# Optimization experiments

Hardware: AMD Instinct MI355X
Metric: run time of the kernel (lower is better)

Reference implementation:

```python
import jax, jax.numpy as jnp
import numpy as np

B, S, F_DIM, FILT = 4096, 41, 128, 128
EPS_BN = 1e-5
EPS_SQ = 1e-21


def squash(v):
    n = jnp.linalg.norm(v, axis=-1, keepdims=True)
    return (1.0 - 1.0 / (jnp.exp(n) + EPS_SQ)) * (v / (n + EPS_SQ))


def position_linear(x, Wstack, bstack, window):
    # x: [B,S,F]; Wstack: [S, window*F, FILT]; bstack: [S, FILT]
    p = window // 2
    Bq, Sq, Fq = x.shape
    xp = jnp.pad(x, ((0, 0), (p, p), (0, 0)))
    idx = jnp.arange(Sq)[:, None] + jnp.arange(window)[None, :]  # [S, window]
    xw = xp[:, idx, :].reshape(Bq, Sq, window * Fq)
    return jax.nn.relu(jnp.einsum('bsf,sfo->bso', xw, Wstack) + bstack[None])


def batchnorm(x, g, b, axes):
    mu = jnp.mean(x, axis=axes, keepdims=True)
    var = jnp.var(x, axis=axes, keepdims=True)
    shape = [1] * x.ndim
    shape[1] = x.shape[1]
    return (x - mu) * jax.lax.rsqrt(var + EPS_BN) * g.reshape(shape) + b.reshape(shape)


def conv1d(x, w, groups=1):
    # x: [N,C,L], w: [O, C//groups, K], padding same (k=3, pad=1)
    return jax.lax.conv_general_dilated(
        x, w, window_strides=(1,), padding=[(1, 1)],
        dimension_numbers=('NCH', 'OIH', 'NCH'), feature_group_count=groups)


def setup_inputs() -> dict:
    key = jax.random.key(0)
    ks = jax.random.split(key, 16)
    sc = lambda fan_in: 1.0 / np.sqrt(fan_in)
    d = {}
    d['x'] = jax.random.randint(ks[0], (B, S), 0, 4, dtype=jnp.int32)
    d['emb'] = jax.random.normal(ks[1], (4, F_DIM), dtype=jnp.float32)
    for i, w in enumerate([3, 5, 7]):
        fin = w * F_DIM
        d[f'W{w}'] = jax.random.uniform(ks[2 + i], (S, fin, FILT), jnp.float32, -sc(fin), sc(fin))
        d[f'b{w}'] = jnp.zeros((S, FILT), jnp.float32)
    d['conv1_w'] = jax.random.uniform(ks[5], (64, 41, 3), jnp.float32, -sc(41 * 3), sc(41 * 3))
    d['conv1_b'] = jnp.zeros((64,), jnp.float32)
    d['bn_g'] = jnp.ones((64,), jnp.float32)
    d['bn_b'] = jnp.zeros((64,), jnp.float32)
    d['caps_w'] = jax.random.uniform(ks[6], (64, 32, 3), jnp.float32, -sc(32 * 3), sc(32 * 3))
    d['caps_b'] = jnp.zeros((64,), jnp.float32)
    d['route_W'] = jax.random.normal(ks[7], (2, 64, F_DIM), jnp.float32)
    d['route_b'] = jnp.zeros((2, 64, 1), jnp.float32)
    d['fc1_w'] = jax.random.uniform(ks[8], (F_DIM, 64), jnp.float32, -sc(F_DIM), sc(F_DIM))
    d['bn1_g'] = jnp.ones((2,), jnp.float32)
    d['bn1_b'] = jnp.zeros((2,), jnp.float32)
    d['fc2_w'] = jax.random.uniform(ks[9], (64, 32), jnp.float32, -sc(64), sc(64))
    d['bn2_g'] = jnp.ones((2,), jnp.float32)
    d['bn2_b'] = jnp.zeros((2,), jnp.float32)
    d['fc3_w'] = jax.random.uniform(ks[10], (32, 1), jnp.float32, -sc(32), sc(32))
    return d


def reference(x, emb, W3, b3, W5, b5, W7, b7, conv1_w, conv1_b, bn_g, bn_b,
              caps_w, caps_b, route_W, route_b,
              fc1_w, bn1_g, bn1_b, fc2_w, bn2_g, bn2_b, fc3_w):
    h = emb[x]                                    # [B,41,128]
    h = position_linear(h, W3, b3, 3)
    h = position_linear(h, W5, b5, 5)
    h = position_linear(h, W7, b7, 7)             # [B,41,128]
    h = conv1d(h, conv1_w) + conv1_b[None, :, None]  # [B,64,128]
    h = jax.nn.relu(batchnorm(h, bn_g, bn_b, axes=(0, 2)))
    h = conv1d(h, caps_w, groups=2) + caps_b[None, :, None]
    h = squash(h)                                 # [B,64,128]
    # Routing layer
    u = h[:, None, :, :] * route_W[None]          # [B,2,64,128]
    c = jnp.sum(u * u, axis=-1, keepdims=True) / jnp.sqrt(128.0)  # [B,2,64,1]
    c = jax.nn.softmax(c, axis=-1)                # softmax over size-1 axis -> ones
    c = c + route_b[None]
    s = squash(jnp.sum(u * c, axis=-2))           # [B,2,128]
    # FC head
    pair = s[:, :, None, :] + s[:, None, :, :]    # [B,2,2,128]
    y = jnp.max(pair, axis=1)                     # [B,2,128]
    y = jax.nn.relu(batchnorm(y @ fc1_w, bn1_g, bn1_b, axes=(0, 2)))
    y = jax.nn.relu(batchnorm(y @ fc2_w, bn2_g, bn2_b, axes=(0, 2)))
    y = jax.nn.sigmoid(y @ fc3_w)                 # [B,2,1]
    return jnp.max(y, axis=1)                     # [B,1]
```

## Files before the change

### kernel.cpp

```cpp
#include <hip/hip_runtime.h>
#include <cstdint>

typedef unsigned short u16;
typedef unsigned int   u32;
typedef __attribute__((ext_vector_type(8))) short bf16x8;
typedef __attribute__((ext_vector_type(4))) float f32x4;

#define DEVFN static __device__ __forceinline__

constexpr int B  = 4096;
constexpr int SQ = 41;

DEVFN float bf2f(u16 v) { return __uint_as_float(((u32)v) << 16); }
DEVFN u16 f2bf(float f) {
  u32 u = __float_as_uint(f);
  u += 0x7fffu + ((u >> 16) & 1u);
  return (u16)(u >> 16);
}
DEVFN u32 pack2(float a, float b) { return (u32)f2bf(a) | ((u32)f2bf(b) << 16); }

DEVFN void gload16(const void* g, void* l) {
  __builtin_amdgcn_global_load_lds(
      (const __attribute__((address_space(1))) unsigned int*)g,
      (__attribute__((address_space(3))) unsigned int*)l, 16, 0, 0);
}

__global__ void k_pack(const float* __restrict__ cw, const float* __restrict__ cpw,
                       const float* __restrict__ rW, const float* __restrict__ rb,
                       u16* __restrict__ wpk, u16* __restrict__ cpk,
                       u16* __restrict__ rwp) {
  int i = blockIdx.x * 256 + threadIdx.x;
  if (i < 12288) {
    int tt = i >> 12, rem = i & 4095, o = rem >> 6, c = rem & 63;
    float v = (c < 41) ? cw[(o * 41 + c) * 3 + tt] : 0.f;
    wpk[(tt * 64 + o) * 64 + (c ^ ((o & 7) << 3))] = f2bf(v);
  } else if (i < 18432) {
    int k = i - 12288;
    int tt = k >> 11, rem = k & 2047, o = rem >> 5, c = rem & 31;
    cpk[(tt * 64 + o) * 32 + (c ^ ((o & 3) << 3))] = f2bf(cpw[(o * 32 + c) * 3 + tt]);
  } else if (i < 34816) {
    int k = i - 18432;
    rwp[k] = f2bf(rW[k] * (1.f + rb[k >> 7]));
  }
}

__global__ void k_combo(const int* __restrict__ x, int* __restrict__ combo) {
  int i = blockIdx.x * 256 + threadIdx.x;
  if (i >= B * SQ) return;
  int b = i / SQ, s = i - b * SQ;
  const int* xb = x + b * SQ;
  int d0 = (s > 0) ? xb[s - 1] : 4;
  int d1 = xb[s];
  int d2 = (s < SQ - 1) ? xb[s + 1] : 4;
  combo[i] = d0 * 25 + d1 * 5 + d2;
}

__global__ void k_gmat(const float* __restrict__ emb, const float* __restrict__ W3,
                       float* __restrict__ G) {
  int s = blockIdx.x / 3, ww = blockIdx.x % 3;
  int o = threadIdx.x;
  const float* Ws = W3 + ((size_t)s * 384 + ww * 128) * 128;
  float a0 = 0.f, a1 = 0.f, a2 = 0.f, a3 = 0.f;
  for (int f = 0; f < 128; ++f) {
    float wg = Ws[(size_t)f * 128 + o];
    a0 = fmaf(emb[f], wg, a0);
    a1 = fmaf(emb[128 + f], wg, a1);
    a2 = fmaf(emb[256 + f], wg, a2);
    a3 = fmaf(emb[384 + f], wg, a3);
  }
  float* Gp = G + ((size_t)(s * 3 + ww) * 5) * 128 + o;
  Gp[0] = a0; Gp[128] = a1; Gp[256] = a2; Gp[384] = a3; Gp[512] = 0.f;
}

__global__ void k_t1(const float* __restrict__ G, const float* __restrict__ b3,
                     float* __restrict__ t1T) {
  int i = blockIdx.x * 256 + threadIdx.x;
  if (i >= SQ * 128 * 125) return;
  int v = i % 125, so = i / 125;
  int s = so >> 7, o = so & 127;
  int d0 = v / 25, r = v % 25;
  int d1 = r / 5, d2 = r % 5;
  float acc = b3[so]
      + G[((size_t)(s * 3 + 0) * 5 + d0) * 128 + o]
      + G[((size_t)(s * 3 + 1) * 5 + d1) * 128 + o]
      + G[((size_t)(s * 3 + 2) * 5 + d2) * 128 + o];
  t1T[i] = fmaxf(acc, 0.f);
}

__global__ __launch_bounds__(128) void k_t2(const float* __restrict__ t1T,
                                            const float* __restrict__ W5,
                                            u16* __restrict__ t2) {
  int bx = blockIdx.x;
  int s = bx / 25; int r = bx % 25;
  int ww = r / 5;  int vt = (r % 5) * 25;
  int o = threadIdx.x;
  int t = s + ww - 2;
  u16* dst = t2 + ((size_t)(s * 5 + ww) * 125 + vt) * 128 + o;
  if (t < 0 || t >= SQ) {
    #pragma unroll
    for (int v = 0; v < 25; ++v) dst[(size_t)v * 128] = 0;
    return;
  }
  float acc[25];
  #pragma unroll
  for (int v = 0; v < 25; ++v) acc[v] = 0.f;
  const float* Ws = W5 + ((size_t)s * 640 + ww * 128) * 128;
  const float* tp = t1T + (size_t)t * 128 * 125 + vt;
  for (int f = 0; f < 128; ++f) {
    float wg = Ws[(size_t)f * 128 + o];
    #pragma unroll
    for (int v = 0; v < 25; ++v) acc[v] = fmaf(tp[f * 125 + v], wg, acc[v]);
  }
  #pragma unroll
  for (int v = 0; v < 25; ++v) dst[(size_t)v * 128] = f2bf(acc[v]);
}

__global__ __launch_bounds__(256) void k_h2(const u16* __restrict__ t2,
                                            const int* __restrict__ combo,
                                            const float* __restrict__ b5,
                                            u16* __restrict__ h2) {
  const int i = blockIdx.x * 256 + threadIdx.x;
  const int o8 = (i & 15) * 8;
  const int rid = i >> 4;
  const int s = rid >> 12, b = rid & 4095;
  float acc[8];
  {
    float4 b0 = *reinterpret_cast<const float4*>(b5 + s * 128 + o8);
    float4 b1 = *reinterpret_cast<const float4*>(b5 + s * 128 + o8 + 4);
    acc[0] = b0.x; acc[1] = b0.y; acc[2] = b0.z; acc[3] = b0.w;
    acc[4] = b1.x; acc[5] = b1.y; acc[6] = b1.z; acc[7] = b1.w;
  }
  const int* cb = combo + b * SQ;
  #pragma unroll
  for (int ww = 0; ww < 5; ++ww) {
    const int t = s + ww - 2;
    if (0 <= t && t < SQ) {
      const int c = cb[t];
      uint4 raw = *reinterpret_cast<const uint4*>(
          t2 + ((size_t)(s * 5 + ww) * 125 + c) * 128 + o8);
      acc[0] += __uint_as_float(raw.x << 16);
      acc[1] += __uint_as_float(raw.x & 0xffff0000u);
      acc[2] += __uint_as_float(raw.y << 16);
      acc[3] += __uint_as_float(raw.y & 0xffff0000u);
      acc[4] += __uint_as_float(raw.z << 16);
      acc[5] += __uint_as_float(raw.z & 0xffff0000u);
      acc[6] += __uint_as_float(raw.w << 16);
      acc[7] += __uint_as_float(raw.w & 0xffff0000u);
    }
  }
  uint4 pk;
  pk.x = pack2(fmaxf(acc[0], 0.f), fmaxf(acc[1], 0.f));
  pk.y = pack2(fmaxf(acc[2], 0.f), fmaxf(acc[3], 0.f));
  pk.z = pack2(fmaxf(acc[4], 0.f), fmaxf(acc[5], 0.f));
  pk.w = pack2(fmaxf(acc[6], 0.f), fmaxf(acc[7], 0.f));
  *reinterpret_cast<uint4*>(h2 + ((size_t)b * SQ + s) * 128 + o8) = pk;
}

__global__ __launch_bounds__(256) void k_w7t(const float* __restrict__ W7,
                                             u16* __restrict__ w7t) {
  __shared__ float tile[64][65];
  const int s = blockIdx.z;
  const int k0 = blockIdx.x * 64;
  const int o0 = blockIdx.y * 64;
  const int t = threadIdx.x;
  #pragma unroll
  for (int i = 0; i < 16; ++i) {
    int idx = t + i * 256;
    int kl = idx >> 6, ol = idx & 63;
    tile[kl][ol] = W7[((size_t)s * 896 + k0 + kl) * 128 + o0 + ol];
  }
  __syncthreads();
  #pragma unroll
  for (int i = 0; i < 16; ++i) {
    int idx = t + i * 256;
    int ol = idx >> 6, kl = idx & 63;
    w7t[((size_t)s * 128 + o0 + ol) * 896 + k0 + kl] = f2bf(tile[kl][ol]);
  }
}

__global__ __launch_bounds__(256) void k_gemm7_mfma(const u16* __restrict__ h2,
                                                    const u16* __restrict__ w7t,
                                                    const float* __restrict__ b7,
                                                    u16* __restrict__ h3) {
  __shared__ u16 As[128 * 64];
  __shared__ u16 Bs[128 * 64];
  const int s  = blockIdx.y;
  const int b0 = blockIdx.x * 128;
  const int t  = threadIdx.x;
  const int lane = t & 63, w = t >> 6;
  const int wr = w >> 1, wc = w & 1;
  const int lcol = lane & 15, qk = lane >> 4;

  f32x4 acc[4][4];
  #pragma unroll
  for (int i = 0; i < 4; ++i)
    #pragma unroll
    for (int j = 0; j < 4; ++j) acc[i][j] = (f32x4){0.f, 0.f, 0.f, 0.f};

  const u16* wbase = w7t + (size_t)s * 128 * 896;

  for (int k0 = 0; k0 < 896; k0 += 64) {
    const int ww = k0 >> 7;
    const int tr = s + ww - 3;
    const int kf0 = k0 & 127;
    if (0 <= tr && tr < SQ) {
      #pragma unroll
      for (int it = 0; it < 4; ++it) {
        const int L = it * 4096 + t * 16;
        const int r = L >> 7;
        const int g = (L >> 4) & 7;
        const int gs = g ^ (r & 7);
        gload16(h2 + ((size_t)(b0 + r) * SQ + tr) * 128 + kf0 + gs * 8,
                (char*)As + it * 4096 + w * 1024);
      }
    } else {
      #pragma unroll
      for (int it = 0; it < 4; ++it)
        *reinterpret_cast<uint4*>((char*)As + it * 4096 + t * 16) =
            make_uint4(0u, 0u, 0u, 0u);
    }
    #pragma unroll
    for (int it = 0; it < 4; ++it) {
      const int L = it * 4096 + t * 16;
      const int o = L >> 7;
      const int g = (L >> 4) & 7;
      const int gs = g ^ (o & 7);
      gload16(wbase + (size_t)o * 896 + k0 + gs * 8,
              (char*)Bs + it * 4096 + w * 1024);
    }
    __syncthreads();
    #pragma unroll
    for (int kk = 0; kk < 2; ++kk) {
      const int gk = kk * 4 + qk;
      bf16x8 av[4], bv[4];
      #pragma unroll
      for (int m = 0; m < 4; ++m) {
        const int zr = wr * 64 + m * 16 + lcol;
        av[m] = *reinterpret_cast<const bf16x8*>(As + zr * 64 + ((gk ^ (zr & 7)) << 3));
      }
      #pragma unroll
      for (int n = 0; n < 4; ++n) {
        const int br = wc * 64 + n * 16 + lcol;
        bv[n] = *reinterpret_cast<const bf16x8*>(Bs + br * 64 + ((gk ^ (br & 7)) << 3));
      }
      #pragma unroll
      for (int m = 0; m < 4; ++m)
        #pragma unroll
        for (int n = 0; n < 4; ++n)
          acc[m][n] = __builtin_amdgcn_mfma_f32_16x16x32_bf16(av[m], bv[n], acc[m][n], 0, 0, 0);
    }
    __syncthreads();
  }

  const int rq = (lane >> 4) * 4;
  #pragma unroll
  for (int n = 0; n < 4; ++n) {
    const int o = wc * 64 + n * 16 + lcol;
    const float bias = b7[s * 128 + o];
    #pragma unroll
    for (int m = 0; m < 4; ++m) {
      #pragma unroll
      for (int rg = 0; rg < 4; ++rg) {
        const int row = b0 + wr * 64 + m * 16 + rq + rg;
        h3[((size_t)row * SQ + s) * 128 + o] = f2bf(fmaxf(acc[m][n][rg] + bias, 0.f));
      }
    }
  }
}

__global__ __launch_bounds__(256) void k_conv1(const u16* __restrict__ h3,
                                               const u16* __restrict__ wpk,
                                               const float* __restrict__ cb,
                                               u16* __restrict__ c1T,
                                               float2* __restrict__ part) {
  __shared__ u16 zs[6144];
  __shared__ u16 zt[130 * 64];
  __shared__ u16 wl[3 * 64 * 64];
  __shared__ float2 red[4][64];
  const int b = blockIdx.x;
  const int t = threadIdx.x;
  const int lane = t & 63, wv = t >> 6;

  const u16* src = h3 + (size_t)b * (SQ * 128);
  #pragma unroll
  for (int it = 0; it < 3; ++it)
    gload16(src + ((size_t)it * 256 + t) * 8, (char*)zs + it * 4096 + wv * 1024);
  #pragma unroll
  for (int it = 0; it < 6; ++it)
    gload16(wpk + ((size_t)it * 256 + t) * 8, (char*)wl + it * 4096 + wv * 1024);

  if (t < 64) zt[t] = 0;
  else if (t < 128) zt[129 * 64 + t - 64] = 0;
  __syncthreads();

  {
    const int l = t & 127, jb = (t >> 7) * 32;
    const int sw = ((l + 1) & 7) << 3;
    u16* dst = zt + (l + 1) * 64;
    #pragma unroll
    for (int j = 0; j < 32; ++j) {
      int c = (jb + j + l) & 63;
      dst[c ^ sw] = (c < 41) ? zs[c * 128 + l] : (u16)0;
    }
  }
  __syncthreads();

  f32x4 acc[2][4];
  #pragma unroll
  for (int m = 0; m < 2; ++m)
    #pragma unroll
    for (int n = 0; n < 4; ++n) acc[m][n] = (f32x4){0.f, 0.f, 0.f, 0.f};
  const int r = lane & 15, kq = (lane >> 4) * 8;

  #pragma unroll
  for (int tt = 0; tt < 3; ++tt) {
    #pragma unroll
    for (int kk = 0; kk < 2; ++kk) {
      const int kof = kk * 32 + kq;
      bf16x8 av[2], bv[4];
      #pragma unroll
      for (int m = 0; m < 2; ++m) {
        const int zr = wv * 32 + m * 16 + r + tt;
        av[m] = *reinterpret_cast<const bf16x8*>(zt + zr * 64 + (kof ^ ((zr & 7) << 3)));
      }
      #pragma unroll
      for (int n = 0; n < 4; ++n) {
        const int o = n * 16 + r;
        bv[n] = *reinterpret_cast<const bf16x8*>(wl + (tt * 64 + o) * 64 + (kof ^ ((o & 7) << 3)));
      }
      #pragma unroll
      for (int m = 0; m < 2; ++m)
        #pragma unroll
        for (int n = 0; n < 4; ++n)
          acc[m][n] = __builtin_amdgcn_mfma_f32_16x16x32_bf16(av[m], bv[n], acc[m][n], 0, 0, 0);
    }
  }

  const int q = lane >> 4;
  u16* outb = c1T + (size_t)b * 8192;
  #pragma unroll
  for (int n = 0; n < 4; ++n) {
    const int o = n * 16 + r;
    const float bias = cb[o];
    float s1 = 0.f, s2 = 0.f;
    #pragma unroll
    for (int m = 0; m < 2; ++m) {
      #pragma unroll
      for (int rg = 0; rg < 4; ++rg) {
        float v = acc[m][n][rg] + bias;
        s1 += v; s2 += v * v;
        outb[(wv * 32 + m * 16 + q * 4 + rg) * 64 + o] = f2bf(v);
      }
    }
    s1 += __shfl_xor(s1, 16); s1 += __shfl_xor(s1, 32);
    s2 += __shfl_xor(s2, 16); s2 += __shfl_xor(s2, 32);
    if (lane < 16) red[wv][n * 16 + lane] = make_float2(s1, s2);
  }
  __syncthreads();
  if (t < 64) {
    float S = red[0][t].x + red[1][t].x + red[2][t].x + red[3][t].x;
    float Q = red[0][t].y + red[1][t].y + red[2][t].y + red[3][t].y;
    part[(size_t)t * B + b] = make_float2(S, Q);
  }
}

__global__ void k_bnfin(const float2* __restrict__ part, const float* __restrict__ g,
                        const float* __restrict__ bb, float* __restrict__ scale,
                        float* __restrict__ shift) {
  int o = blockIdx.x;
  float s = 0.f, q = 0.f;
  for (int i = threadIdx.x; i < B; i += 256) {
    float2 p = part[(size_t)o * B + i];
    s += p.x; q += p.y;
  }
  #pragma unroll
  for (int off = 32; off; off >>= 1) { s += __shfl_down(s, off); q += __shfl_down(q, off); }
  __shared__ float rs[4], rq[4];
  int wv = threadIdx.x >> 6, ln = threadIdx.x & 63;
  if (ln == 0) { rs[wv] = s; rq[wv] = q; }
  __syncthreads();
  if (threadIdx.x == 0) {
    float S = rs[0] + rs[1] + rs[2] + rs[3];
    float Q = rq[0] + rq[1] + rq[2] + rq[3];
    const float n = (float)B * 128.f;
    float mu = S / n, var = Q / n - mu * mu;
    float sc = g[o] * rsqrtf(var + 1e-5f);
    scale[o] = sc; shift[o] = bb[o] - mu * sc;
  }
}

constexpr int NB = 8;
__global__ __launch_bounds__(256) void k_caps(const u16* __restrict__ c1T,
                                              const float* __restrict__ scale,
                                              const float* __restrict__ shift,
                                              const u16* __restrict__ cpk,
                                              const float* __restrict__ cpb,
                                              const u16* __restrict__ rwp,
                                              const float* __restrict__ f1,
                                              float* __restrict__ y1) {
  __shared__ u16 zt[130 * 64];
  __shared__ u16 wl[3 * 64 * 32];
  __shared__ float f1l[128 * 64];
  __shared__ float red[4][64];
  __shared__ float fl[64];
  __shared__ float sc_s[64], sh_s[64];
  __shared__ float red2[4][2];
  __shared__ float yl[2][128];
  __shared__ float pt[128];
  const int b0 = blockIdx.x * NB;
  const int t = threadIdx.x;
  const int lane = t & 63, wv = t >> 6;
  const int r = lane & 15, kq = (lane >> 4) * 8, q = lane >> 4;

  #pragma unroll
  for (int it = 0; it < 3; ++it)
    gload16(cpk + ((size_t)it * 256 + t) * 8, (char*)wl + it * 4096 + wv * 1024);
  #pragma unroll
  for (int it = 0; it < 8; ++it)
    gload16(f1 + ((size_t)it * 256 + t) * 4, (char*)f1l + it * 4096 + wv * 1024);
  if (t < 64) { sc_s[t] = scale[t]; sh_s[t] = shift[t]; }
  if (t < 64) zt[t] = 0;
  else if (t < 128) zt[129 * 64 + t - 64] = 0;

  uint4 raw[4], rawn[4];
  {
    const u16* src = c1T + (size_t)b0 * 8192;
    #pragma unroll
    for (int p = 0; p < 4; ++p)
      raw[p] = *reinterpret_cast<const uint4*>(src + ((size_t)t + p * 256) * 8);
  }

  for (int i = 0; i < NB; ++i) {
    const int b = b0 + i;
    __syncthreads();

    #pragma unroll
    for (int p = 0; p < 4; ++p) {
      int idx = t + p * 256;
      int l = idx >> 3, c0 = (idx & 7) * 8;
      float vv[8];
      vv[0] = __uint_as_float(raw[p].x << 16); vv[1] = __uint_as_float(raw[p].x & 0xffff0000u);
      vv[2] = __uint_as_float(raw[p].y << 16); vv[3] = __uint_as_float(raw[p].y & 0xffff0000u);
      vv[4] = __uint_as_float(raw[p].z << 16); vv[5] = __uint_as_float(raw[p].z & 0xffff0000u);
      vv[6] = __uint_as_float(raw[p].w << 16); vv[7] = __uint_as_float(raw[p].w & 0xffff0000u);
      float a0 = fmaxf(fmaf(vv[0], sc_s[c0 + 0], sh_s[c0 + 0]), 0.f);
      float a1 = fmaxf(fmaf(vv[1], sc_s[c0 + 1], sh_s[c0 + 1]), 0.f);
      float a2 = fmaxf(fmaf(vv[2], sc_s[c0 + 2], sh_s[c0 + 2]), 0.f);
      float a3 = fmaxf(fmaf(vv[3], sc_s[c0 + 3], sh_s[c0 + 3]), 0.f);
      float a4 = fmaxf(fmaf(vv[4], sc_s[c0 + 4], sh_s[c0 + 4]), 0.f);
      float a5 = fmaxf(fmaf(vv[5], sc_s[c0 + 5], sh_s[c0 + 5]), 0.f);
      float a6 = fmaxf(fmaf(vv[6], sc_s[c0 + 6], sh_s[c0 + 6]), 0.f);
      float a7 = fmaxf(fmaf(vv[7], sc_s[c0 + 7], sh_s[c0 + 7]), 0.f);
      uint4 pk;
      pk.x = pack2(a0, a1); pk.y = pack2(a2, a3);
      pk.z = pack2(a4, a5); pk.w = pack2(a6, a7);
      *reinterpret_cast<uint4*>(zt + (l + 1) * 64 + (c0 ^ (((l + 1) & 7) << 3))) = pk;
    }
    if (i + 1 < NB) {
      const u16* srcn = c1T + (size_t)(b + 1) * 8192;
      #pragma unroll
      for (int p = 0; p < 4; ++p)
        rawn[p] = *reinterpret_cast<const uint4*>(srcn + ((size_t)t + p * 256) * 8);
    }
    __syncthreads();

    f32x4 acc[2][4];
    #pragma unroll
    for (int m = 0; m < 2; ++m)
      #pragma unroll
      for (int n = 0; n < 4; ++n) acc[m][n] = (f32x4){0.f, 0.f, 0.f, 0.f};
    #pragma unroll
    for (int tt = 0; tt < 3; ++tt) {
      bf16x8 av[2][2], bv[4];
      #pragma unroll
      for (int m = 0; m < 2; ++m) {
        const int zr = wv * 32 + m * 16 + r + tt;
        const int sw = (zr & 7) << 3;
        av[m][0] = *reinterpret_cast<const bf16x8*>(zt + zr * 64 + (kq ^ sw));
        av[m][1] = *reinterpret_cast<const bf16x8*>(zt + zr * 64 + ((32 + kq) ^ sw));
      }
      #pragma unroll
      for (int n = 0; n < 4; ++n) {
        const int o = n * 16 + r;
        bv[n] = *reinterpret_cast<const bf16x8*>(wl + (tt * 64 + o) * 32 + (kq ^ ((o & 3) << 3)));
      }
      #pragma unroll
      for (int m = 0; m < 2; ++m)
        #pragma unroll
        for (int n = 0; n < 4; ++n)
          acc[m][n] = __builtin_amdgcn_mfma_f32_16x16x32_bf16(av[m][n >> 1], bv[n], acc[m][n], 0, 0, 0);
    }

    #pragma unroll
    for (int n = 0; n < 4; ++n) {
      const int o = n * 16 + r;
      const float bias = cpb[o];
      float s2 = 0.f;
      #pragma unroll
      for (int m = 0; m < 2; ++m) {
        #pragma unroll
        for (int rg = 0; rg < 4; ++rg) {
          float v = acc[m][n][rg] + bias;
          acc[m][n][rg] = v;
          s2 += v * v;
        }
      }
      s2 += __shfl_xor(s2, 16); s2 += __shfl_xor(s2, 32);
      if (lane < 16) red[wv][n * 16 + lane] = s2;
    }
    __syncthreads();
    if (t < 64) {
      float S = red[0][t] + red[1][t] + red[2][t] + red[3][t];
      float nn = sqrtf(S);
      fl[t] = (1.f - 1.f / (expf(nn) + 1e-21f)) / (nn + 1e-21f);
    }
    __syncthreads();

    float s0[2][4], s1[2][4];
    #pragma unroll
    for (int m = 0; m < 2; ++m)
      #pragma unroll
      for (int rg = 0; rg < 4; ++rg) { s0[m][rg] = 0.f; s1[m][rg] = 0.f; }
    #pragma unroll
    for (int n = 0; n < 4; ++n) {
      const int o = n * 16 + r;
      const float fact = fl[o];
      #pragma unroll
      for (int m = 0; m < 2; ++m) {
        const int l0 = wv * 32 + m * 16 + q * 4;
        uint2 rw0 = *reinterpret_cast<const uint2*>(rwp + (size_t)o * 128 + l0);
        uint2 rw1 = *reinterpret_cast<const uint2*>(rwp + (size_t)(64 + o) * 128 + l0);
        #pragma unroll
        for (int rg = 0; rg < 4; ++rg) {
          float v = acc[m][n][rg] * fact;
          u32 w0w = (rg < 2) ? rw0.x : rw0.y;
          u32 w1w = (rg < 2) ? rw1.x : rw1.y;
          float w0 = __uint_as_float((rg & 1) ? (w0w & 0xffff0000u) : (w0w << 16));
          float w1 = __uint_as_float((rg & 1) ? (w1w & 0xffff0000u) : (w1w << 16));
          s0[m][rg] = fmaf(v, w0, s0[m][rg]);
          s1[m][rg] = fmaf(v, w1, s1[m][rg]);
        }
      }
    }
    #pragma unroll
    for (int m = 0; m < 2; ++m)
      #pragma unroll
      for (int rg = 0; rg < 4; ++rg) {
        #pragma unroll
        for (int off = 1; off <= 8; off <<= 1) {
          s0[m][rg] += __shfl_xor(s0[m][rg], off);
          s1[m][rg] += __shfl_xor(s1[m][rg], off);
        }
      }
    float n0 = 0.f, n1 = 0.f;
    #pragma unroll
    for (int m = 0; m < 2; ++m)
      #pragma unroll
      for (int rg = 0; rg < 4; ++rg) {
        n0 = fmaf(s0[m][rg], s0[m][rg], n0);
        n1 = fmaf(s1[m][rg], s1[m][rg], n1);
      }
    n0 += __shfl_xor(n0, 16); n0 += __shfl_xor(n0, 32);
    n1 += __shfl_xor(n1, 16); n1 += __shfl_xor(n1, 32);
    if (lane == 0) { red2[wv][0] = n0; red2[wv][1] = n1; }
    __syncthreads();
    {
      float t0 = red2[0][0] + red2[1][0] + red2[2][0] + red2[3][0];
      float t1 = red2[0][1] + red2[1][1] + red2[2][1] + red2[3][1];
      float nn0 = sqrtf(t0), nn1 = sqrtf(t1);
      float fa0 = (1.f - 1.f / (expf(nn0) + 1e-21f)) / (nn0 + 1e-21f);
      float fa1 = (1.f - 1.f / (expf(nn1) + 1e-21f)) / (nn1 + 1e-21f);
      if (r == 0) {
        #pragma unroll
        for (int m = 0; m < 2; ++m)
          #pragma unroll
          for (int rg = 0; rg < 4; ++rg) {
            float v0 = s0[m][rg] * fa0, v1 = s1[m][rg] * fa1;
            float mx = fmaxf(v0, v1);
            int l = wv * 32 + m * 16 + q * 4 + rg;
            yl[0][l] = v0 + mx;
            yl[1][l] = v1 + mx;
          }
      }
    }
    __syncthreads();

    {
      const int h = t >> 7, idx = t & 127;
      const int jj = idx >> 6, qq = idx & 63;
      float a = 0.f;
      const float* yrow = &yl[jj][h * 64];
      const float* frow = f1l + (h * 64) * 64 + qq;
      #pragma unroll 8
      for (int tt = 0; tt < 64; ++tt)
        a = fmaf(yrow[tt], frow[tt * 64], a);
      if (h == 1) pt[idx] = a;
      __syncthreads();
      if (h == 0)
        y1[((size_t)b * 2 + jj) * 64 + qq] = a + pt[idx];
    }

    #pragma unroll
    for (int p = 0; p < 4; ++p) raw[p] = rawn[p];
  }
}

__global__ __launch_bounds__(256) void k_bnstat_part(const float* __restrict__ y,
                                                     float2* __restrict__ pp,
                                                     int perShift) {
  const int jj = blockIdx.y;
  const int per = 1 << perShift;
  const int n4 = (B << perShift) >> 2;
  const int p4shift = perShift - 2;
  const int p4mask = (per >> 2) - 1;
  float s = 0.f, q = 0.f;
  for (int i = blockIdx.x * 256 + threadIdx.x; i < n4; i += 64 * 256) {
    int bI = i >> p4shift, c4 = (i & p4mask) * 4;
    float4 v = *reinterpret_cast<const float4*>(
        y + (size_t)bI * (per * 2) + jj * per + c4);
    s += v.x + v.y + v.z + v.w;
    q += v.x * v.x + v.y * v.y + v.z * v.z + v.w * v.w;
  }
  #pragma unroll
  for (int off = 32; off; off >>= 1) { s += __shfl_down(s, off); q += __shfl_down(q, off); }
  __shared__ float rs[4], rq[4];
  int wv = threadIdx.x >> 6, ln = threadIdx.x & 63;
  if (ln == 0) { rs[wv] = s; rq[wv] = q; }
  __syncthreads();
  if (threadIdx.x == 0)
    pp[jj * 64 + blockIdx.x] =
        make_float2(rs[0] + rs[1] + rs[2] + rs[3], rq[0] + rq[1] + rq[2] + rq[3]);
}

__global__ void k_bnstat_fin(const float2* __restrict__ pp, const float* __restrict__ g,
                             const float* __restrict__ bb, float* __restrict__ scale,
                             float* __restrict__ shift, int perShift) {
  const int jj = blockIdx.x;
  float2 p = pp[jj * 64 + threadIdx.x];
  float s = p.x, q = p.y;
  #pragma unroll
  for (int off = 32; off; off >>= 1) { s += __shfl_down(s, off); q += __shfl_down(q, off); }
  if (threadIdx.x == 0) {
    float fn = (float)(B << perShift);
    float mu = s / fn, var = q / fn - mu * mu;
    float sc = g[jj] * rsqrtf(var + 1e-5f);
    scale[jj] = sc; shift[jj] = bb[jj] - mu * sc;
  }
}

__global__ void k_fc2(const float* __restrict__ y1, const float* __restrict__ sc1,
                      const float* __restrict__ sh1, const float* __restrict__ f2,
                      float* __restrict__ y2) {
  int t = threadIdx.x;
  int b = blockIdx.x * 4 + (t >> 6);
  int jj = (t >> 5) & 1, r = t & 31;
  float sc = sc1[jj], sh = sh1[jj];
  const float* yb = y1 + (size_t)b * 128 + jj * 64;
  float acc = 0.f;
  for (int q = 0; q < 64; ++q) {
    float v = fmaxf(fmaf(yb[q], sc, sh), 0.f);
    acc = fmaf(v, f2[q * 32 + r], acc);
  }
  y2[(size_t)b * 64 + jj * 32 + r] = acc;
}

__global__ void k_head(const float* __restrict__ y2, const float* __restrict__ sc2,
                       const float* __restrict__ sh2, const float* __restrict__ f3,
                       float* __restrict__ out) {
  int b = blockIdx.x * 256 + threadIdx.x;
  if (b >= B) return;
  const float* yb = y2 + (size_t)b * 64;
  float c0 = sc2[0], d0 = sh2[0], c1v = sc2[1], d1 = sh2[1];
  float a0 = 0.f, a1 = 0.f;
  for (int r = 0; r < 32; ++r) {
    float w = f3[r];
    a0 = fmaf(fmaxf(fmaf(yb[r], c0, d0), 0.f), w, a0);
    a1 = fmaf(fmaxf(fmaf(yb[32 + r], c1v, d1), 0.f), w, a1);
  }
  float s0 = 1.f / (1.f + expf(-a0));
  float s1 = 1.f / (1.f + expf(-a1));
  out[b] = fmaxf(s0, s1);
}

constexpr size_t SZ_H2    = (size_t)B * SQ * 128 * 2;
constexpr size_t SZ_C1    = (size_t)B * 64 * 128 * 2;
constexpr size_t OFF_H2   = 0;
constexpr size_t OFF_H3   = SZ_H2;
constexpr size_t R1       = 2 * SZ_H2;
constexpr size_t OFF_G    = R1;
constexpr size_t OFF_T1   = OFF_G + 314880;
constexpr size_t OFF_T2   = OFF_T1 + 2624000;
constexpr size_t OFF_CMB  = OFF_T2 + 6560000;
constexpr size_t OFF_W7T  = OFF_CMB + 671744;
constexpr size_t OFF_C1   = R1;
constexpr size_t R2       = R1 + SZ_C1;
constexpr size_t OFF_PART = R2;
constexpr size_t OFF_Y1   = OFF_PART + 2097152;
constexpr size_t OFF_Y2   = OFF_Y1 + 2097152;
constexpr size_t OFF_SM   = OFF_Y2 + 1048576;
constexpr size_t OFF_BNP  = OFF_SM + 1024;
constexpr size_t OFF_WPK  = OFF_BNP + 1024;
constexpr size_t OFF_CPK  = OFF_WPK + 24576;
constexpr size_t OFF_RWP  = OFF_CPK + 12288;

extern "C" void kernel_launch(void* const* d_in, const int* in_sizes, int n_in,
                              void* d_out, int out_size, void* d_ws, size_t ws_size,
                              hipStream_t stream) {
  const int*   x   = (const int*)d_in[0];
  const float* emb = (const float*)d_in[1];
  const float* W3  = (const float*)d_in[2];
  const float* b3  = (const float*)d_in[3];
  const float* W5  = (const float*)d_in[4];
  const float* b5  = (const float*)d_in[5];
  const float* W7  = (const float*)d_in[6];
  const float* b7  = (const float*)d_in[7];
  const float* c1w = (const float*)d_in[8];
  const float* c1b = (const float*)d_in[9];
  const float* bng = (const float*)d_in[10];
  const float* bnb = (const float*)d_in[11];
  const float* cpw = (const float*)d_in[12];
  const float* cpb = (const float*)d_in[13];
  const float* rW  = (const float*)d_in[14];
  const float* rb  = (const float*)d_in[15];
  const float* f1  = (const float*)d_in[16];
  const float* g1  = (const float*)d_in[17];
  const float* bb1 = (const float*)d_in[18];
  const float* f2  = (const float*)d_in[19];
  const float* g2  = (const float*)d_in[20];
  const float* bb2 = (const float*)d_in[21];
  const float* f3  = (const float*)d_in[22];

  char* wsb = (char*)d_ws;
  u16*    h2p   = (u16*)(wsb + OFF_H2);
  u16*    h3p   = (u16*)(wsb + OFF_H3);
  float*  Gp    = (float*)(wsb + OFF_G);
  float*  t1p   = (float*)(wsb + OFF_T1);
  u16*    t2p   = (u16*)(wsb + OFF_T2);
  int*    cmbp  = (int*)(wsb + OFF_CMB);
  u16*    w7tp  = (u16*)(wsb + OFF_W7T);
  u16*    c1p   = (u16*)(wsb + OFF_C1);
  float2* partp = (float2*)(wsb + OFF_PART);
  float*  y1p   = (float*)(wsb + OFF_Y1);
  float*  y2p   = (float*)(wsb + OFF_Y2);
  float*  scp   = (float*)(wsb + OFF_SM);
  float*  shp   = scp + 64;
  float*  sc1p  = shp + 64;
  float*  sh1p  = sc1p + 2;
  float*  sc2p  = sh1p + 2;
  float*  sh2p  = sc2p + 2;
  float2* bnpp  = (float2*)(wsb + OFF_BNP);
  u16*    wpkp  = (u16*)(wsb + OFF_WPK);
  u16*    cpkp  = (u16*)(wsb + OFF_CPK);
  u16*    rwpp  = (u16*)(wsb + OFF_RWP);

  k_pack<<<136, 256, 0, stream>>>(c1w, cpw, rW, rb, wpkp, cpkp, rwpp);
  k_combo<<<(B * SQ + 255) / 256, 256, 0, stream>>>(x, cmbp);
  k_w7t<<<dim3(14, 2, SQ), 256, 0, stream>>>(W7, w7tp);
  k_gmat<<<SQ * 3, 128, 0, stream>>>(emb, W3, Gp);
  k_t1<<<(SQ * 128 * 125 + 255) / 256, 256, 0, stream>>>(Gp, b3, t1p);
  k_t2<<<SQ * 25, 128, 0, stream>>>(t1p, W5, t2p);
  k_h2<<<(B * SQ * 16) / 256, 256, 0, stream>>>(t2p, cmbp, b5, h2p);
  k_gemm7_mfma<<<dim3(32, SQ), 256, 0, stream>>>(h2p, w7tp, b7, h3p);
  k_conv1<<<B, 256, 0, stream>>>(h3p, wpkp, c1b, c1p, partp);
  k_bnfin<<<64, 256, 0, stream>>>(partp, bng, bnb, scp, shp);
  k_caps<<<B / NB, 256, 0, stream>>>(c1p, scp, shp, cpkp, cpb, rwpp, f1, y1p);
  k_bnstat_part<<<dim3(64, 2), 256, 0, stream>>>(y1p, bnpp, 6);
  k_bnstat_fin<<<2, 64, 0, stream>>>(bnpp, g1, bb1, sc1p, sh1p, 6);
  k_fc2<<<B / 4, 256, 0, stream>>>(y1p, sc1p, sh1p, f2, y2p);
  k_bnstat_part<<<dim3(64, 2), 256, 0, stream>>>(y2p, bnpp, 5);
  k_bnstat_fin<<<2, 64, 0, stream>>>(bnpp, g2, bb2, sc2p, sh2p, 5);
  k_head<<<B / 256, 256, 0, stream>>>(y2p, sc2p, sh2p, f3, (float*)d_out);
}
```

Before: 244.7 us.

## Double-buffer LDS in position-7 GEMM and remap blocks across XCDs

```diff
diff --git a/kernel.cpp b/kernel.cpp
--- a/kernel.cpp
+++ b/kernel.cpp
@@ -182,11 +182,13 @@
                                                     const u16* __restrict__ w7t,
                                                     const float* __restrict__ b7,
                                                     u16* __restrict__ h3) {
-  __shared__ u16 As[128 * 64];
-  __shared__ u16 Bs[128 * 64];
-  const int s  = blockIdx.y;
-  const int b0 = blockIdx.x * 128;
-  const int t  = threadIdx.x;
+  __shared__ u16 As[2][8192];
+  __shared__ u16 Bs[2][8192];
+  const int bid  = blockIdx.x;
+  const int orig = (bid & 7) * 164 + (bid >> 3);
+  const int s    = orig >> 5;
+  const int b0   = (orig & 31) * 128;
+  const int t    = threadIdx.x;
   const int lane = t & 63, w = t >> 6;
   const int wr = w >> 1, wc = w & 1;
   const int lcol = lane & 15, qk = lane >> 4;
@@ -199,10 +201,10 @@
 
   const u16* wbase = w7t + (size_t)s * 128 * 896;
 
-  for (int k0 = 0; k0 < 896; k0 += 64) {
-    const int ww = k0 >> 7;
-    const int tr = s + ww - 3;
-    const int kf0 = k0 & 127;
+  auto stage = [&](int kt, int bi) -> int {
+    const int k0 = kt * 64;
+    const int ww = k0 >> 7, tr = s + ww - 3, kf0 = k0 & 127;
+    int issued = 0;
     if (0 <= tr && tr < SQ) {
       #pragma unroll
       for (int it = 0; it < 4; ++it) {
@@ -211,12 +213,13 @@
         const int g = (L >> 4) & 7;
         const int gs = g ^ (r & 7);
         gload16(h2 + ((size_t)(b0 + r) * SQ + tr) * 128 + kf0 + gs * 8,
-                (char*)As + it * 4096 + w * 1024);
-      }
+                (char*)As[bi] + it * 4096 + w * 1024);
+      }
+      issued += 4;
     } else {
       #pragma unroll
       for (int it = 0; it < 4; ++it)
-        *reinterpret_cast<uint4*>((char*)As + it * 4096 + t * 16) =
+        *reinterpret_cast<uint4*>((char*)As[bi] + it * 4096 + t * 16) =
             make_uint4(0u, 0u, 0u, 0u);
     }
     #pragma unroll
@@ -226,9 +229,25 @@
       const int g = (L >> 4) & 7;
       const int gs = g ^ (o & 7);
       gload16(wbase + (size_t)o * 896 + k0 + gs * 8,
-              (char*)Bs + it * 4096 + w * 1024);
-    }
-    __syncthreads();
+              (char*)Bs[bi] + it * 4096 + w * 1024);
+    }
+    return issued + 4;
+  };
+
+  stage(0, 0);
+
+  for (int kt = 0; kt < 14; ++kt) {
+    const int cur = kt & 1;
+    int ni = 0;
+    if (kt < 13) ni = stage(kt + 1, cur ^ 1);
+    if (ni == 8)      asm volatile("s_waitcnt vmcnt(8) lgkmcnt(0)" ::: "memory");
+    else if (ni == 4) asm volatile("s_waitcnt vmcnt(4) lgkmcnt(0)" ::: "memory");
+    else              asm volatile("s_waitcnt vmcnt(0) lgkmcnt(0)" ::: "memory");
+    __builtin_amdgcn_sched_barrier(0);
+    __builtin_amdgcn_s_barrier();
+
+    const u16* Ac = As[cur];
+    const u16* Bc = Bs[cur];
     #pragma unroll
     for (int kk = 0; kk < 2; ++kk) {
       const int gk = kk * 4 + qk;
@@ -236,12 +255,12 @@
       #pragma unroll
       for (int m = 0; m < 4; ++m) {
         const int zr = wr * 64 + m * 16 + lcol;
-        av[m] = *reinterpret_cast<const bf16x8*>(As + zr * 64 + ((gk ^ (zr & 7)) << 3));
+        av[m] = *reinterpret_cast<const bf16x8*>(Ac + zr * 64 + ((gk ^ (zr & 7)) << 3));
       }
       #pragma unroll
       for (int n = 0; n < 4; ++n) {
         const int br = wc * 64 + n * 16 + lcol;
-        bv[n] = *reinterpret_cast<const bf16x8*>(Bs + br * 64 + ((gk ^ (br & 7)) << 3));
+        bv[n] = *reinterpret_cast<const bf16x8*>(Bc + br * 64 + ((gk ^ (br & 7)) << 3));
       }
       #pragma unroll
       for (int m = 0; m < 4; ++m)
@@ -249,7 +268,7 @@
         for (int n = 0; n < 4; ++n)
           acc[m][n] = __builtin_amdgcn_mfma_f32_16x16x32_bf16(av[m], bv[n], acc[m][n], 0, 0, 0);
     }
-    __syncthreads();
+    __builtin_amdgcn_s_barrier();
   }
 
   const int rq = (lane >> 4) * 4;
@@ -760,7 +779,7 @@
   k_t1<<<(SQ * 128 * 125 + 255) / 256, 256, 0, stream>>>(Gp, b3, t1p);
   k_t2<<<SQ * 25, 128, 0, stream>>>(t1p, W5, t2p);
   k_h2<<<(B * SQ * 16) / 256, 256, 0, stream>>>(t2p, cmbp, b5, h2p);
-  k_gemm7_mfma<<<dim3(32, SQ), 256, 0, stream>>>(h2p, w7tp, b7, h3p);
+  k_gemm7_mfma<<<1312, 256, 0, stream>>>(h2p, w7tp, b7, h3p);
   k_conv1<<<B, 256, 0, stream>>>(h3p, wpkp, c1b, c1p, partp);
   k_bnfin<<<64, 256, 0, stream>>>(partp, bng, bnb, scp, shp);
   k_caps<<<B / NB, 256, 0, stream>>>(c1p, scp, shp, cpkp, cpb, rwpp, f1, y1p);
```

New measurement: 247.3 us. Within noise of the previous version (+1.1%).

## Multi-stage pipeline the W7 GEMM with a 4-deep async LDS ring buffer

Applied to the files above, without the earlier changes.

```diff
diff --git a/kernel.cpp b/kernel.cpp
--- a/kernel.cpp
+++ b/kernel.cpp
@@ -28,7 +28,7 @@
 __global__ void k_pack(const float* __restrict__ cw, const float* __restrict__ cpw,
                        const float* __restrict__ rW, const float* __restrict__ rb,
                        u16* __restrict__ wpk, u16* __restrict__ cpk,
-                       u16* __restrict__ rwp) {
+                       u16* __restrict__ rwp, u16* __restrict__ zp) {
   int i = blockIdx.x * 256 + threadIdx.x;
   if (i < 12288) {
     int tt = i >> 12, rem = i & 4095, o = rem >> 6, c = rem & 63;
@@ -41,6 +41,8 @@
   } else if (i < 34816) {
     int k = i - 18432;
     rwp[k] = f2bf(rW[k] * (1.f + rb[k >> 7]));
+  } else if (i < 38912) {
+    zp[i - 34816] = 0;
   }
 }
 
@@ -181,9 +183,10 @@
 __global__ __launch_bounds__(256) void k_gemm7_mfma(const u16* __restrict__ h2,
                                                     const u16* __restrict__ w7t,
                                                     const float* __restrict__ b7,
+                                                    const u16* __restrict__ zp,
                                                     u16* __restrict__ h3) {
-  __shared__ u16 As[128 * 64];
-  __shared__ u16 Bs[128 * 64];
+  __shared__ u16 As[4][4096];
+  __shared__ u16 Bs[4][4096];
   const int s  = blockIdx.y;
   const int b0 = blockIdx.x * 128;
   const int t  = threadIdx.x;
@@ -199,57 +202,58 @@
 
   const u16* wbase = w7t + (size_t)s * 128 * 896;
 
-  for (int k0 = 0; k0 < 896; k0 += 64) {
-    const int ww = k0 >> 7;
-    const int tr = s + ww - 3;
-    const int kf0 = k0 & 127;
-    if (0 <= tr && tr < SQ) {
-      #pragma unroll
-      for (int it = 0; it < 4; ++it) {
-        const int L = it * 4096 + t * 16;
-        const int r = L >> 7;
-        const int g = (L >> 4) & 7;
-        const int gs = g ^ (r & 7);
-        gload16(h2 + ((size_t)(b0 + r) * SQ + tr) * 128 + kf0 + gs * 8,
-                (char*)As + it * 4096 + w * 1024);
-      }
-    } else {
-      #pragma unroll
-      for (int it = 0; it < 4; ++it)
-        *reinterpret_cast<uint4*>((char*)As + it * 4096 + t * 16) =
-            make_uint4(0u, 0u, 0u, 0u);
-    }
-    #pragma unroll
-    for (int it = 0; it < 4; ++it) {
+  auto stage = [&](int kt, int bi) {
+    const int ww = kt >> 2, tr = s + ww - 3;
+    const int kf0 = (kt & 3) * 32;
+    const bool val = (0 <= tr && tr < SQ);
+    #pragma unroll
+    for (int it = 0; it < 2; ++it) {
       const int L = it * 4096 + t * 16;
-      const int o = L >> 7;
-      const int g = (L >> 4) & 7;
-      const int gs = g ^ (o & 7);
-      gload16(wbase + (size_t)o * 896 + k0 + gs * 8,
-              (char*)Bs + it * 4096 + w * 1024);
-    }
-    __syncthreads();
-    #pragma unroll
-    for (int kk = 0; kk < 2; ++kk) {
-      const int gk = kk * 4 + qk;
-      bf16x8 av[4], bv[4];
-      #pragma unroll
-      for (int m = 0; m < 4; ++m) {
-        const int zr = wr * 64 + m * 16 + lcol;
-        av[m] = *reinterpret_cast<const bf16x8*>(As + zr * 64 + ((gk ^ (zr & 7)) << 3));
-      }
-      #pragma unroll
-      for (int n = 0; n < 4; ++n) {
-        const int br = wc * 64 + n * 16 + lcol;
-        bv[n] = *reinterpret_cast<const bf16x8*>(Bs + br * 64 + ((gk ^ (br & 7)) << 3));
-      }
-      #pragma unroll
-      for (int m = 0; m < 4; ++m)
-        #pragma unroll
-        for (int n = 0; n < 4; ++n)
-          acc[m][n] = __builtin_amdgcn_mfma_f32_16x16x32_bf16(av[m], bv[n], acc[m][n], 0, 0, 0);
-    }
-    __syncthreads();
+      const int r = L >> 6, g = (L >> 4) & 3;
+      const u16* src = val
+          ? h2 + ((size_t)(b0 + r) * SQ + tr) * 128 + kf0 + ((g ^ (r & 3)) << 3)
+          : zp + (L >> 1);
+      gload16(src, (char*)As[bi] + it * 4096 + w * 1024);
+    }
+    #pragma unroll
+    for (int it = 0; it < 2; ++it) {
+      const int L = it * 4096 + t * 16;
+      const int o = L >> 6, g = (L >> 4) & 3;
+      gload16(wbase + (size_t)o * 896 + kt * 32 + ((g ^ (o & 3)) << 3),
+              (char*)Bs[bi] + it * 4096 + w * 1024);
+    }
+  };
+
+  stage(0, 0); stage(1, 1); stage(2, 2);
+
+  for (int kt = 0; kt < 28; ++kt) {
+    __builtin_amdgcn_sched_barrier(0);
+    if (kt + 3 < 28) stage(kt + 3, (kt + 3) & 3);
+    if (kt < 25)       asm volatile("s_waitcnt vmcnt(12)" ::: "memory");
+    else if (kt == 25) asm volatile("s_waitcnt vmcnt(8)" ::: "memory");
+    else if (kt == 26) asm volatile("s_waitcnt vmcnt(4)" ::: "memory");
+    else               asm volatile("s_waitcnt vmcnt(0)" ::: "memory");
+    __builtin_amdgcn_s_barrier();
+    __builtin_amdgcn_sched_barrier(0);
+    const int bi = kt & 3;
+    bf16x8 av[4], bv[4];
+    #pragma unroll
+    for (int m = 0; m < 4; ++m) {
+      const int zr = wr * 64 + m * 16 + lcol;
+      av[m] = *reinterpret_cast<const bf16x8*>(&As[bi][zr * 32 + ((qk ^ (zr & 3)) << 3)]);
+    }
+    #pragma unroll
+    for (int n = 0; n < 4; ++n) {
+      const int br = wc * 64 + n * 16 + lcol;
+      bv[n] = *reinterpret_cast<const bf16x8*>(&Bs[bi][br * 32 + ((qk ^ (br & 3)) << 3)]);
+    }
+    #pragma unroll
+    for (int m = 0; m < 4; ++m)
+      #pragma unroll
+      for (int n = 0; n < 4; ++n)
+        acc[m][n] = __builtin_amdgcn_mfma_f32_16x16x32_bf16(av[m], bv[n], acc[m][n], 0, 0, 0);
+    __builtin_amdgcn_sched_barrier(0);
+    __builtin_amdgcn_s_barrier();
   }
 
   const int rq = (lane >> 4) * 4;
@@ -692,6 +696,7 @@
 constexpr size_t OFF_T2   = OFF_T1 + 2624000;
 constexpr size_t OFF_CMB  = OFF_T2 + 6560000;
 constexpr size_t OFF_W7T  = OFF_CMB + 671744;
+constexpr size_t OFF_ZP   = OFF_W7T + 9404416;
 constexpr size_t OFF_C1   = R1;
 constexpr size_t R2       = R1 + SZ_C1;
 constexpr size_t OFF_PART = R2;
@@ -738,6 +743,7 @@
   u16*    t2p   = (u16*)(wsb + OFF_T2);
   int*    cmbp  = (int*)(wsb + OFF_CMB);
   u16*    w7tp  = (u16*)(wsb + OFF_W7T);
+  u16*    zpp   = (u16*)(wsb + OFF_ZP);
   u16*    c1p   = (u16*)(wsb + OFF_C1);
   float2* partp = (float2*)(wsb + OFF_PART);
   float*  y1p   = (float*)(wsb + OFF_Y1);
@@ -753,14 +759,14 @@
   u16*    cpkp  = (u16*)(wsb + OFF_CPK);
   u16*    rwpp  = (u16*)(wsb + OFF_RWP);
 
-  k_pack<<<136, 256, 0, stream>>>(c1w, cpw, rW, rb, wpkp, cpkp, rwpp);
+  k_pack<<<152, 256, 0, stream>>>(c1w, cpw, rW, rb, wpkp, cpkp, rwpp, zpp);
   k_combo<<<(B * SQ + 255) / 256, 256, 0, stream>>>(x, cmbp);
   k_w7t<<<dim3(14, 2, SQ), 256, 0, stream>>>(W7, w7tp);
   k_gmat<<<SQ * 3, 128, 0, stream>>>(emb, W3, Gp);
   k_t1<<<(SQ * 128 * 125 + 255) / 256, 256, 0, stream>>>(Gp, b3, t1p);
   k_t2<<<SQ * 25, 128, 0, stream>>>(t1p, W5, t2p);
   k_h2<<<(B * SQ * 16) / 256, 256, 0, stream>>>(t2p, cmbp, b5, h2p);
-  k_gemm7_mfma<<<dim3(32, SQ), 256, 0, stream>>>(h2p, w7tp, b7, h3p);
+  k_gemm7_mfma<<<dim3(32, SQ), 256, 0, stream>>>(h2p, w7tp, b7, zpp, h3p);
   k_conv1<<<B, 256, 0, stream>>>(h3p, wpkp, c1b, c1p, partp);
   k_bnfin<<<64, 256, 0, stream>>>(partp, bng, bnb, scp, shp);
   k_caps<<<B / NB, 256, 0, stream>>>(c1p, scp, shp, cpkp, cpb, rwpp, f1, y1p);
```

Result: slower. 260.0 us (+6.2%).
